# Optimization experiments

Measured on AMD Instinct MI355X. Metric: run time of the kernel, lower is better.

The kernel has to match this reference:

```python
import jax, jax.numpy as jnp
import numpy as np

THETA = 1.0       # thr
TAU_RHO = 0.5     # grad_width
SCALE_RHO = 1.0   # grad_scale


def avg_pool4(x):
    # x: (N, C, H, W, T) -> 4x4 average pool per timestep (pool weight = 1/16)
    N, C, H, W, T = x.shape
    return x.reshape(N, C, H // 4, 4, W // 4, 4, T).mean(axis=(3, 5))


def conv2d_t(x, w):
    # SLAYER conv: spatial-only conv3d with kernel (k,k,1), pad 3, no bias.
    # x: (N, C, H, W, T), w: (O, I, 7, 7)
    N, C, H, W, T = x.shape
    xt = jnp.moveaxis(x, -1, 1).reshape(N * T, C, H, W)
    y = jax.lax.conv_general_dilated(
        xt, w, window_strides=(1, 1), padding=[(3, 3), (3, 3)],
        dimension_numbers=('NCHW', 'OIHW', 'NCHW'))
    O = w.shape[0]
    return jnp.moveaxis(y.reshape(N, T, O, H, W), 1, -1)


def psp(x):
    # IAF SRM kernel = unit step (Ts=1) -> causal cumulative sum over time
    return jnp.cumsum(x, axis=-1)


def _spike_scan(u):
    # Sequential threshold + persistent refractory subtraction (scaleRef=1, IAF)
    uT = jnp.moveaxis(u, -1, 0)  # (T, ...)
    def step(r, ut):
        v = ut + r                       # membrane incl. refractory
        s = (v >= THETA).astype(u.dtype)
        return r - THETA * s, (s, v)
    _, (sT, vT) = jax.lax.scan(step, jnp.zeros_like(uT[0]), uT)
    return jnp.moveaxis(sT, 0, -1), jnp.moveaxis(vT, 0, -1)


@jax.custom_vjp
def spike(u):
    return _spike_scan(u)[0]


def _spike_fwd(u):
    s, v = _spike_scan(u)
    return s, v


def _spike_bwd(v, g):
    # SLAYER surrogate: no BPTT through refractory recurrence
    pdf = (SCALE_RHO / TAU_RHO) * jnp.exp(-jnp.abs(v - THETA) / TAU_RHO)
    return (g * pdf,)


spike.defvjp(_spike_fwd, _spike_bwd)


def setup_inputs() -> dict:
    key = jax.random.key(0)
    k0, k1, k2, k3 = jax.random.split(key, 4)
    data = jax.random.uniform(k0, (4, 2, 256, 256, 100), dtype=jnp.float32)
    w0 = jax.random.normal(k1, (4, 2, 7, 7), dtype=jnp.float32) * 0.1
    w1 = jax.random.normal(k2, (8, 4, 7, 7), dtype=jnp.float32) * 0.05
    wl = jax.random.normal(k3, (2, 8, 4, 4), dtype=jnp.float32) * 0.1
    return {"data": data, "w0": w0, "w1": w1, "wl": wl}


def reference(data, w0, w1, wl):
    x = avg_pool4(data)                      # (N,2,64,64,T)
    x = spike(psp(conv2d_t(x, w0)))          # (N,4,64,64,T)
    x = avg_pool4(x)                         # (N,4,16,16,T)
    x = spike(psp(conv2d_t(x, w1)))          # (N,8,16,16,T)
    x = avg_pool4(x)                         # (N,8,4,4,T)
    out = jnp.einsum('nchwt,ochw->not', x, wl)  # dense (4,4,8)->2, squeeze
    return out                               # (N,2,T)
```

## Files before the change

kernel.cpp:

```cpp
#include <hip/hip_runtime.h>
#include <hip/hip_bf16.h>

using u16 = unsigned short;
using u32 = unsigned int;
using u64 = unsigned long long;

__device__ __forceinline__ float b2f(u16 u){
  union { u32 i; float f; } x; x.i = ((u32)u) << 16; return x.f;
}

__global__ __launch_bounds__(256) void k_prep(const void* __restrict__ data,
                                              const void* __restrict__ w0,
                                              const void* __restrict__ w1,
                                              const void* __restrict__ wl,
                                              int* __restrict__ gflag,
                                              float* __restrict__ w0f,
                                              float* __restrict__ w1f,
                                              float* __restrict__ wlf){
  __shared__ int zs[4], ss[4];
  __shared__ int sflag;
  int tid = threadIdx.x;
  u32 w = ((const u32*)data)[tid];
  u16 lo = (u16)(w & 0xFFFFu);
  u64 zb = __ballot(lo == 0);
  u64 sb = __ballot((lo >> 15) & 1);
  int wave = tid >> 6;
  if((tid & 63) == 0){ zs[wave] = __popcll(zb); ss[wave] = __popcll(sb); }
  __syncthreads();
  if(tid == 0){
    int zeros = zs[0]+zs[1]+zs[2]+zs[3];
    int signs = ss[0]+ss[1]+ss[2]+ss[3];
    int f = (zeros >= 128 || signs > 0) ? 1 : 0;
    sflag = f; *gflag = f;
  }
  __syncthreads();
  int f = sflag;
  const float* w0F = (const float*)w0; const u16* w0H = (const u16*)w0;
  const float* w1F = (const float*)w1; const u16* w1H = (const u16*)w1;
  const float* wlF = (const float*)wl; const u16* wlH = (const u16*)wl;
  for(int i = tid; i < 392;  i += 256) w0f[i] = f ? w0F[i] : b2f(w0H[i]);
  for(int i = tid; i < 1568; i += 256) w1f[i] = f ? w1F[i] : b2f(w1H[i]);
  for(int i = tid; i < 256;  i += 256) wlf[i] = f ? wlF[i] : b2f(wlH[i]);
}

__global__ __launch_bounds__(256) void k_pool1(const void* __restrict__ data,
                                               const int* __restrict__ gflag,
                                               float* __restrict__ P1){
  int idx = blockIdx.x * 256 + threadIdx.x;
  int tc  = idx % 25;
  int pix = idx / 25;
  int ow  = pix & 63;
  int oh  = (pix >> 6) & 63;
  int nc  = pix >> 12;
  int t0  = tc * 4;
  size_t off = ((size_t)((nc*256 + oh*4)*256 + ow*4)) * 100 + t0;
  double s0=0.0, s1=0.0, s2=0.0, s3=0.0;
  if(*gflag){
    const float* base = (const float*)data + off;
    #pragma unroll
    for(int di=0; di<4; ++di)
      #pragma unroll
      for(int dj=0; dj<4; ++dj){
        float4 v = *reinterpret_cast<const float4*>(base + (size_t)(di*256 + dj)*100);
        s0 += (double)v.x; s1 += (double)v.y; s2 += (double)v.z; s3 += (double)v.w;
      }
  } else {
    const u16* base = (const u16*)data + off;
    #pragma unroll
    for(int di=0; di<4; ++di)
      #pragma unroll
      for(int dj=0; dj<4; ++dj){
        ushort4 v = *reinterpret_cast<const ushort4*>(base + (size_t)(di*256 + dj)*100);
        s0 += (double)b2f(v.x); s1 += (double)b2f(v.y);
        s2 += (double)b2f(v.z); s3 += (double)b2f(v.w);
      }
  }
  float* o = P1 + (size_t)pix * 100 + t0;
  o[0] = (float)(s0 * 0.0625); o[1] = (float)(s1 * 0.0625);
  o[2] = (float)(s2 * 0.0625); o[3] = (float)(s3 * 0.0625);
}

__global__ __launch_bounds__(256) void k_conv1(const float* __restrict__ P1,
                                               const float* __restrict__ w0f,
                                               double* __restrict__ A1){
  __shared__ float4  tile[968];
  __shared__ double4 wl4[98];
  int bid  = blockIdx.x;
  int tcl  = bid % 25; int rest = bid / 25;
  int tl   = rest & 15; int n = rest >> 4;
  int ty   = (tl >> 2) * 16, tx = (tl & 3) * 16;
  int t0   = tcl * 4;
  int tid  = threadIdx.x;
  for(int i = tid; i < 392; i += 256){
    int o = i / 98, r = i % 98;
    ((double*)wl4)[r*4 + o] = (double)w0f[i];
  }
  for(int idx = tid; idx < 968; idx += 256){
    int ci = idx / 484, r = idx % 484;
    int yy = r / 22, xx = r % 22;
    int gy = ty + yy - 3, gx = tx + xx - 3;
    float4 v; v.x = v.y = v.z = v.w = 0.f;
    if(gy >= 0 && gy < 64 && gx >= 0 && gx < 64){
      const float* p = P1 + ((size_t)((n*2+ci)*64 + gy)*64 + gx)*100 + t0;
      v.x = p[0]; v.y = p[1]; v.z = p[2]; v.w = p[3];
    }
    tile[idx] = v;
  }
  __syncthreads();
  int y = tid >> 4, x = tid & 15;
  double acc[4][4] = {};
  for(int ci = 0; ci < 2; ++ci)
    for(int dy = 0; dy < 7; ++dy){
      #pragma unroll
      for(int dx = 0; dx < 7; ++dx){
        float4 iv = tile[ci*484 + (y+dy)*22 + (x+dx)];
        double4 wv = wl4[ci*49 + dy*7 + dx];
        double i0 = (double)iv.x, i1 = (double)iv.y, i2 = (double)iv.z, i3 = (double)iv.w;
        acc[0][0] += wv.x*i0; acc[0][1] += wv.x*i1; acc[0][2] += wv.x*i2; acc[0][3] += wv.x*i3;
        acc[1][0] += wv.y*i0; acc[1][1] += wv.y*i1; acc[1][2] += wv.y*i2; acc[1][3] += wv.y*i3;
        acc[2][0] += wv.z*i0; acc[2][1] += wv.z*i1; acc[2][2] += wv.z*i2; acc[2][3] += wv.z*i3;
        acc[3][0] += wv.w*i0; acc[3][1] += wv.w*i1; acc[3][2] += wv.w*i2; acc[3][3] += wv.w*i3;
      }
    }
  size_t obase = ((size_t)(n*4)*100 + t0)*4096 + (size_t)(ty+y)*64 + (tx+x);
  #pragma unroll
  for(int o = 0; o < 4; ++o)
    #pragma unroll
    for(int tt = 0; tt < 4; ++tt)
      A1[obase + ((size_t)o*100 + tt)*4096] = acc[o][tt];
}

__global__ __launch_bounds__(64) void k_scan1(const double* __restrict__ A1,
                                              float* __restrict__ S1p){
  int bid = blockIdx.x;
  int xg  = bid & 3, yg = (bid >> 2) & 15, no = bid >> 6;
  int lane = threadIdx.x;
  int lx = lane & 15, ly = lane >> 4;
  int row = yg*4 + ly, col = xg*16 + lx;
  const double* base = A1 + (size_t)no*100*4096 + (size_t)row*64 + col;
  float* outb = S1p + (size_t)no*100*256 + yg*16 + xg*4;
  int cell = lx >> 2;
  u64 cmask = 0x000F000F000F000FULL << (4*cell);
  bool writer = (ly == 0) && ((lx & 3) == 0);
  double u = 0.0, r = 0.0;
  double c0 = base[0], c1 = base[4096], c2 = base[8192], c3 = base[12288];
  for(int tb = 0; tb < 25; ++tb){
    int nb = (tb + 1 < 25) ? tb + 1 : 24;
    const double* pn = base + (size_t)nb*4*4096;
    double n0 = pn[0], n1 = pn[4096], n2 = pn[8192], n3 = pn[12288];
    #pragma unroll
    for(int j = 0; j < 4; ++j){
      double a = (j==0)?c0:(j==1)?c1:(j==2)?c2:c3;
      u += a;
      bool sp = (u + r >= 1.0);
      if(sp) r -= 1.0;
      u64 m = __ballot(sp);
      if(writer){
        float cnt = (float)__popcll(m & cmask);
        outb[(size_t)(tb*4 + j)*256 + cell] = cnt * 0.0625f;
      }
    }
    c0 = n0; c1 = n1; c2 = n2; c3 = n3;
  }
}

__global__ __launch_bounds__(256) void k_conv2(const float* __restrict__ S1p,
                                               const float* __restrict__ w1f,
                                               double* __restrict__ A2){
  __shared__ float   tf[4*4*484];
  __shared__ double4 wl4[196];
  int bid = blockIdx.x;
  int oh  = bid & 1; int rest = bid >> 1;
  int tc  = rest % 25; int n = rest / 25;
  int t0  = tc * 4;
  int tid = threadIdx.x;
  for(int i = tid; i < 7744; i += 256) tf[i] = 0.f;
  for(int i = tid; i < 784; i += 256){
    int oj = i / 196, rem = i % 196;
    ((double*)wl4)[rem*4 + oj] = (double)w1f[(oh*4 + oj)*196 + rem];
  }
  __syncthreads();
  for(int i = tid; i < 4096; i += 256){
    int ci = i >> 10, tt = (i >> 8) & 3, p = i & 255;
    int yy = p >> 4, xx = p & 15;
    tf[(ci*4 + tt)*484 + (yy+3)*22 + (xx+3)] =
        S1p[((size_t)(n*4+ci)*100 + t0 + tt)*256 + p];
  }
  __syncthreads();
  int y = tid >> 4, x = tid & 15;
  double acc[4][4] = {};
  for(int ci = 0; ci < 4; ++ci)
    for(int dy = 0; dy < 7; ++dy){
      #pragma unroll
      for(int dx = 0; dx < 7; ++dx){
        const float* tp = &tf[ci*1936 + (y+dy)*22 + (x+dx)];
        double4 wv = wl4[ci*49 + dy*7 + dx];
        double i0 = (double)tp[0],   i1 = (double)tp[484];
        double i2 = (double)tp[968], i3 = (double)tp[1452];
        acc[0][0] += wv.x*i0; acc[0][1] += wv.x*i1; acc[0][2] += wv.x*i2; acc[0][3] += wv.x*i3;
        acc[1][0] += wv.y*i0; acc[1][1] += wv.y*i1; acc[1][2] += wv.y*i2; acc[1][3] += wv.y*i3;
        acc[2][0] += wv.z*i0; acc[2][1] += wv.z*i1; acc[2][2] += wv.z*i2; acc[2][3] += wv.z*i3;
        acc[3][0] += wv.w*i0; acc[3][1] += wv.w*i1; acc[3][2] += wv.w*i2; acc[3][3] += wv.w*i3;
      }
    }
  size_t obase = ((size_t)(n*8 + oh*4)*100 + t0)*256 + tid;
  #pragma unroll
  for(int oj = 0; oj < 4; ++oj)
    #pragma unroll
    for(int tt = 0; tt < 4; ++tt)
      A2[obase + ((size_t)oj*100 + tt)*256] = acc[oj][tt];
}

__global__ __launch_bounds__(64) void k_scan2(const double* __restrict__ A2,
                                              const float* __restrict__ wlf,
                                              float* __restrict__ P4){
  int bid  = blockIdx.x;
  int q    = bid & 3, nc = bid >> 2, c = nc & 7;
  int lane = threadIdx.x;
  int px   = q*64 + lane;
  float w0g[4], w1g[4];
  #pragma unroll
  for(int g = 0; g < 4; ++g){
    w0g[g] = wlf[      c*16 + q*4 + g] * 0.0625f;
    w1g[g] = wlf[128 + c*16 + q*4 + g] * 0.0625f;
  }
  const double* base = A2 + (size_t)nc*100*256 + px;
  float* outb = P4 + (size_t)bid * 200;
  double u = 0.0, r = 0.0;
  double c0 = base[0], c1 = base[256], c2 = base[512], c3 = base[768];
  for(int tb = 0; tb < 25; ++tb){
    int nb = (tb + 1 < 25) ? tb + 1 : 24;
    const double* pn = base + (size_t)nb*4*256;
    double n0 = pn[0], n1 = pn[256], n2 = pn[512], n3 = pn[768];
    #pragma unroll
    for(int j = 0; j < 4; ++j){
      double a = (j==0)?c0:(j==1)?c1:(j==2)?c2:c3;
      u += a;
      bool sp = (u + r >= 1.0);
      if(sp) r -= 1.0;
      u64 m = __ballot(sp);
      if(lane == 0){
        float p0 = 0.f, p1 = 0.f;
        #pragma unroll
        for(int g = 0; g < 4; ++g){
          float cnt = (float)__popcll(m & (0x000F000F000F000FULL << (4*g)));
          p0 += cnt * w0g[g]; p1 += cnt * w1g[g];
        }
        int t = tb*4 + j;
        outb[t] = p0; outb[100 + t] = p1;
      }
    }
    c0 = n0; c1 = n1; c2 = n2; c3 = n3;
  }
}

__global__ __launch_bounds__(256) void k_out(const float* __restrict__ P4,
                                             const int* __restrict__ gflag,
                                             void* __restrict__ out){
  int idx = blockIdx.x * 256 + threadIdx.x;
  if(idx >= 800) return;
  int t = idx % 100; int o = (idx / 100) & 1; int n = idx / 200;
  float s = 0.f;
  for(int cq = 0; cq < 32; ++cq)
    s += P4[((size_t)(n*32 + cq))*200 + o*100 + t];
  if(*gflag) ((float*)out)[idx] = s;
  else       ((__hip_bfloat16*)out)[idx] = __float2bfloat16(s);
}

extern "C" void kernel_launch(void* const* d_in, const int* in_sizes, int n_in,
                              void* d_out, int out_size, void* d_ws, size_t ws_size,
                              hipStream_t stream) {
  const void* data = d_in[0];
  const void* w0   = d_in[1];
  const void* w1   = d_in[2];
  const void* wl   = d_in[3];
  char* ws = (char*)d_ws;
  float*  P1   = (float*) (ws + 0);
  double* A1   = (double*)(ws + 13107200);
  float*  S1p  = (float*) (ws + 65536000);
  int*    gflag= (int*)   (ws + 67174400);
  float*  w0f  = (float*) (ws + 67174404);
  float*  w1f  = (float*) (ws + 67175972);
  float*  wlf  = (float*) (ws + 67182244);
  double* A2   = (double*)(ws + 0);
  float*  P4   = (float*) (ws + 6553600);

  hipLaunchKernelGGL(k_prep,  dim3(1),    dim3(256), 0, stream,
                     data, w0, w1, wl, gflag, w0f, w1f, wlf);
  hipLaunchKernelGGL(k_pool1, dim3(3200), dim3(256), 0, stream, data, gflag, P1);
  hipLaunchKernelGGL(k_conv1, dim3(1600), dim3(256), 0, stream, P1, w0f, A1);
  hipLaunchKernelGGL(k_scan1, dim3(1024), dim3(64),  0, stream, A1, S1p);
  hipLaunchKernelGGL(k_conv2, dim3(200),  dim3(256), 0, stream, S1p, w1f, A2);
  hipLaunchKernelGGL(k_scan2, dim3(128),  dim3(64),  0, stream, A2, wlf, P4);
  hipLaunchKernelGGL(k_out,   dim3(4),    dim3(256), 0, stream, P4, gflag, d_out);
}
```

Before: 398.0 us.

## Store conv outputs as fp32 float4 in scan-friendly tiled layout

The conv1 and conv2 outputs are now stored as float instead of double. Each group of four timesteps is packed into one float4, laid out so that each scan block reads one contiguous 64-lane chunk per step. This halves intermediate memory traffic and gives coalesced vector loads in the scan kernels, with two-step-ahead prefetch. The cost is that conv accumulations are rounded to fp32 before the scan, which can flip spikes near the threshold.

```diff
diff --git a/kernel.cpp b/kernel.cpp
--- a/kernel.cpp
+++ b/kernel.cpp
@@ -82,7 +82,7 @@
 
 __global__ __launch_bounds__(256) void k_conv1(const float* __restrict__ P1,
                                                const float* __restrict__ w0f,
-                                               double* __restrict__ A1){
+                                               float* __restrict__ A1f){
   __shared__ float4  tile[968];
   __shared__ double4 wl4[98];
   int bid  = blockIdx.x;
@@ -122,35 +122,38 @@
         acc[3][0] += wv.w*i0; acc[3][1] += wv.w*i1; acc[3][2] += wv.w*i2; acc[3][3] += wv.w*i3;
       }
     }
-  size_t obase = ((size_t)(n*4)*100 + t0)*4096 + (size_t)(ty+y)*64 + (tx+x);
+  int stile = (((ty + y) >> 2) << 2) + (tx >> 4);
+  int lane  = ((y & 3) << 4) + x;
+  float4* O = (float4*)A1f;
+  size_t ob = ((size_t)(n*4)*64 + stile) * 25;
+  ob = (ob + tcl) * 64 + lane;
   #pragma unroll
   for(int o = 0; o < 4; ++o)
-    #pragma unroll
-    for(int tt = 0; tt < 4; ++tt)
-      A1[obase + ((size_t)o*100 + tt)*4096] = acc[o][tt];
-}
-
-__global__ __launch_bounds__(64) void k_scan1(const double* __restrict__ A1,
+    O[ob + (size_t)o * 102400] = make_float4((float)acc[o][0], (float)acc[o][1],
+                                             (float)acc[o][2], (float)acc[o][3]);
+}
+
+__global__ __launch_bounds__(64) void k_scan1(const float* __restrict__ A1f,
                                               float* __restrict__ S1p){
-  int bid = blockIdx.x;
-  int xg  = bid & 3, yg = (bid >> 2) & 15, no = bid >> 6;
+  int bid  = blockIdx.x;
+  int stile = bid & 63, no = bid >> 6;
+  int xg = stile & 3, yg = stile >> 2;
   int lane = threadIdx.x;
-  int lx = lane & 15, ly = lane >> 4;
-  int row = yg*4 + ly, col = xg*16 + lx;
-  const double* base = A1 + (size_t)no*100*4096 + (size_t)row*64 + col;
+  int lx = lane & 15;
+  const float4* base = (const float4*)A1f + (size_t)bid * 1600 + lane;
   float* outb = S1p + (size_t)no*100*256 + yg*16 + xg*4;
   int cell = lx >> 2;
   u64 cmask = 0x000F000F000F000FULL << (4*cell);
-  bool writer = (ly == 0) && ((lx & 3) == 0);
+  bool writer = (lane < 16) && ((lx & 3) == 0);
   double u = 0.0, r = 0.0;
-  double c0 = base[0], c1 = base[4096], c2 = base[8192], c3 = base[12288];
+  float4 cur = base[0];
+  float4 nxt = base[64];
   for(int tb = 0; tb < 25; ++tb){
-    int nb = (tb + 1 < 25) ? tb + 1 : 24;
-    const double* pn = base + (size_t)nb*4*4096;
-    double n0 = pn[0], n1 = pn[4096], n2 = pn[8192], n3 = pn[12288];
+    int nb = (tb + 2 < 25) ? tb + 2 : 24;
+    float4 nn = base[(size_t)nb * 64];
     #pragma unroll
     for(int j = 0; j < 4; ++j){
-      double a = (j==0)?c0:(j==1)?c1:(j==2)?c2:c3;
+      double a = (j==0)?(double)cur.x:(j==1)?(double)cur.y:(j==2)?(double)cur.z:(double)cur.w;
       u += a;
       bool sp = (u + r >= 1.0);
       if(sp) r -= 1.0;
@@ -160,13 +163,13 @@
         outb[(size_t)(tb*4 + j)*256 + cell] = cnt * 0.0625f;
       }
     }
-    c0 = n0; c1 = n1; c2 = n2; c3 = n3;
+    cur = nxt; nxt = nn;
   }
 }
 
 __global__ __launch_bounds__(256) void k_conv2(const float* __restrict__ S1p,
                                                const float* __restrict__ w1f,
-                                               double* __restrict__ A2){
+                                               float* __restrict__ A2f){
   __shared__ float   tf[4*4*484];
   __shared__ double4 wl4[196];
   int bid = blockIdx.x;
@@ -203,15 +206,15 @@
         acc[3][0] += wv.w*i0; acc[3][1] += wv.w*i1; acc[3][2] += wv.w*i2; acc[3][3] += wv.w*i3;
       }
     }
-  size_t obase = ((size_t)(n*8 + oh*4)*100 + t0)*256 + tid;
+  float4* O = (float4*)A2f;
+  size_t ob = ((size_t)(n*8 + oh*4)*25 + tc)*256 + tid;
   #pragma unroll
   for(int oj = 0; oj < 4; ++oj)
-    #pragma unroll
-    for(int tt = 0; tt < 4; ++tt)
-      A2[obase + ((size_t)oj*100 + tt)*256] = acc[oj][tt];
-}
-
-__global__ __launch_bounds__(64) void k_scan2(const double* __restrict__ A2,
+    O[ob + (size_t)oj*6400] = make_float4((float)acc[oj][0], (float)acc[oj][1],
+                                          (float)acc[oj][2], (float)acc[oj][3]);
+}
+
+__global__ __launch_bounds__(64) void k_scan2(const float* __restrict__ A2f,
                                               const float* __restrict__ wlf,
                                               float* __restrict__ P4){
   int bid  = blockIdx.x;
@@ -224,17 +227,17 @@
     w0g[g] = wlf[      c*16 + q*4 + g] * 0.0625f;
     w1g[g] = wlf[128 + c*16 + q*4 + g] * 0.0625f;
   }
-  const double* base = A2 + (size_t)nc*100*256 + px;
+  const float4* base = (const float4*)A2f + (size_t)nc*6400 + px;
   float* outb = P4 + (size_t)bid * 200;
   double u = 0.0, r = 0.0;
-  double c0 = base[0], c1 = base[256], c2 = base[512], c3 = base[768];
+  float4 cur = base[0];
+  float4 nxt = base[256];
   for(int tb = 0; tb < 25; ++tb){
-    int nb = (tb + 1 < 25) ? tb + 1 : 24;
-    const double* pn = base + (size_t)nb*4*256;
-    double n0 = pn[0], n1 = pn[256], n2 = pn[512], n3 = pn[768];
+    int nb = (tb + 2 < 25) ? tb + 2 : 24;
+    float4 nn = base[(size_t)nb * 256];
     #pragma unroll
     for(int j = 0; j < 4; ++j){
-      double a = (j==0)?c0:(j==1)?c1:(j==2)?c2:c3;
+      double a = (j==0)?(double)cur.x:(j==1)?(double)cur.y:(j==2)?(double)cur.z:(double)cur.w;
       u += a;
       bool sp = (u + r >= 1.0);
       if(sp) r -= 1.0;
@@ -250,7 +253,7 @@
         outb[t] = p0; outb[100 + t] = p1;
       }
     }
-    c0 = n0; c1 = n1; c2 = n2; c3 = n3;
+    cur = nxt; nxt = nn;
   }
 }
 
@@ -276,21 +279,21 @@
   const void* wl   = d_in[3];
   char* ws = (char*)d_ws;
   float*  P1   = (float*) (ws + 0);
-  double* A1   = (double*)(ws + 13107200);
-  float*  S1p  = (float*) (ws + 65536000);
-  int*    gflag= (int*)   (ws + 67174400);
-  float*  w0f  = (float*) (ws + 67174404);
-  float*  w1f  = (float*) (ws + 67175972);
-  float*  wlf  = (float*) (ws + 67182244);
-  double* A2   = (double*)(ws + 0);
-  float*  P4   = (float*) (ws + 6553600);
+  float*  A1f  = (float*) (ws + 13107200);
+  float*  S1p  = (float*) (ws + 39321600);
+  int*    gflag= (int*)   (ws + 40960000);
+  float*  w0f  = (float*) (ws + 40960004);
+  float*  w1f  = (float*) (ws + 40961572);
+  float*  wlf  = (float*) (ws + 40967844);
+  float*  A2f  = (float*) (ws + 0);
+  float*  P4   = (float*) (ws + 3276800);
 
   hipLaunchKernelGGL(k_prep,  dim3(1),    dim3(256), 0, stream,
                      data, w0, w1, wl, gflag, w0f, w1f, wlf);
   hipLaunchKernelGGL(k_pool1, dim3(3200), dim3(256), 0, stream, data, gflag, P1);
-  hipLaunchKernelGGL(k_conv1, dim3(1600), dim3(256), 0, stream, P1, w0f, A1);
-  hipLaunchKernelGGL(k_scan1, dim3(1024), dim3(64),  0, stream, A1, S1p);
-  hipLaunchKernelGGL(k_conv2, dim3(200),  dim3(256), 0, stream, S1p, w1f, A2);
-  hipLaunchKernelGGL(k_scan2, dim3(128),  dim3(64),  0, stream, A2, wlf, P4);
+  hipLaunchKernelGGL(k_conv1, dim3(1600), dim3(256), 0, stream, P1, w0f, A1f);
+  hipLaunchKernelGGL(k_scan1, dim3(1024), dim3(64),  0, stream, A1f, S1p);
+  hipLaunchKernelGGL(k_conv2, dim3(200),  dim3(256), 0, stream, S1p, w1f, A2f);
+  hipLaunchKernelGGL(k_scan2, dim3(128),  dim3(64),  0, stream, A2f, wlf, P4);
   hipLaunchKernelGGL(k_out,   dim3(4),    dim3(256), 0, stream, P4, gflag, d_out);
 }
```

New measurement: 389.2 us, median of 2. -2.2%, faster.
